# Kernel tuning notes

Hardware: AMD Instinct MI355X
Metric: run time of the kernel (lower is better)

Reference implementation:

```python
import jax, jax.numpy as jnp
import numpy as np

N, C_IN, C_OUT, C_REL, T, V = 64, 256, 256, 32, 64, 25

def conv1x1(x, w, b):
    # x: (n, ci, a, b), w: (co, ci), b: (co,) -> (n, co, a, b)
    return jnp.einsum('oc,ncab->noab', w, x) + b[None, :, None, None]

def setup_inputs() -> dict:
    key = jax.random.key(0)
    ks = jax.random.split(key, 10)
    s_in = 1.0 / np.sqrt(C_IN)
    s_rel = 1.0 / np.sqrt(C_REL)
    return {
        'x': jax.random.normal(ks[0], (N, C_IN, T, V), dtype=jnp.float32),
        'A': jax.random.normal(ks[1], (V, V), dtype=jnp.float32),
        'w1': jax.random.uniform(ks[2], (C_REL, C_IN), jnp.float32, -s_in, s_in),
        'b1': jax.random.uniform(ks[3], (C_REL,), jnp.float32, -s_in, s_in),
        'w2': jax.random.uniform(ks[4], (C_REL, C_IN), jnp.float32, -s_in, s_in),
        'b2': jax.random.uniform(ks[5], (C_REL,), jnp.float32, -s_in, s_in),
        'w3': jax.random.uniform(ks[6], (C_OUT, C_IN), jnp.float32, -s_in, s_in),
        'b3': jax.random.uniform(ks[7], (C_OUT,), jnp.float32, -s_in, s_in),
        'w4': jax.random.uniform(ks[8], (C_OUT, C_REL), jnp.float32, -s_rel, s_rel),
        'b4': jax.random.uniform(ks[9], (C_OUT,), jnp.float32, -s_rel, s_rel),
        'threhold': 0,
        'alpha': 1,
    }

def reference(x, A, w1, b1, w2, b2, w3, b3, w4, b4, threhold, alpha):
    # x: (n, c, t, v)
    # pooled 1x1 convs: fold the T-mean before the channel mix (linear ops commute)
    xm = x.mean(-2)                                   # (n, c, v)
    x1 = jnp.einsum('oc,ncv->nov', w1, xm) + b1[None, :, None]   # (n, r, v)
    x2 = jnp.einsum('oc,ncv->nov', w2, xm) + b2[None, :, None]   # (n, r, v)
    x3 = conv1x1(x, w3, b3)                           # (n, co, t, v)
    # channel-wise affinity: outer difference + tanh -> (n, r, v, v)
    aff = jnp.tanh(x1[:, :, :, None] - x2[:, :, None, :])
    # 1x1 conv over rel channels, scale, add adjacency
    attn = jnp.einsum('or,nruv->nouv', w4, aff) + b4[None, :, None, None]
    attn = attn * alpha + A[None, None]               # (n, co, v, v)
    # graph conv contraction
    out = jnp.einsum('ncuv,nctu->nctv', attn, x3)     # (n, co, t, v)
    return out
```

## Files before the change

kernel.cpp:

```cpp
#include <hip/hip_runtime.h>

#define N_  64
#define CI  256
#define CO  256
#define CR  32
#define T_  64
#define V_  25
#define TV  (T_*V_)
#define VV  (V_*V_)
#define ATS 640

typedef __attribute__((ext_vector_type(8))) short bshort8;
typedef __attribute__((ext_vector_type(4))) float f32x4;

__device__ inline unsigned short f2bf(float f) {
    unsigned int u = __float_as_uint(f);
    return (unsigned short)((u + 0x7FFFu + ((u >> 16) & 1u)) >> 16);
}

__global__ __launch_bounds__(256) void k_mean_cvt(const float* __restrict__ x,
                                                  const float* __restrict__ w3,
                                                  const float* __restrict__ w4,
                                                  float* __restrict__ xm,
                                                  unsigned short* __restrict__ w3f,
                                                  unsigned short* __restrict__ w4f) {
    int b = blockIdx.x;
    int tid = threadIdx.x;
    if (b < 1024) {
        __shared__ float L[16 * 400];
        int n = b >> 4, c0 = (b & 15) * 16;
        float a0 = 0.f, a1 = 0.f;
        for (int ch = 0; ch < 4; ++ch) {
            for (int i = 0; i < 7; ++i) {
                int task = i * 256 + tid;
                if (task < 1600) {
                    int c = task / 100, f4 = task % 100;
                    *(float4*)&L[c * 400 + f4 * 4] =
                        *(const float4*)(x + (size_t)(n * CI + c0 + c) * TV + ch * 400 + f4 * 4);
                }
            }
            __syncthreads();
            {
                int c = tid / 25, v = tid % 25;
                float s = 0.f;
                #pragma unroll
                for (int tl = 0; tl < 16; ++tl) s += L[c * 400 + tl * 25 + v];
                a0 += s;
            }
            if (tid < 144) {
                int oi = tid + 256;
                int c = oi / 25, v = oi % 25;
                float s = 0.f;
                #pragma unroll
                for (int tl = 0; tl < 16; ++tl) s += L[c * 400 + tl * 25 + v];
                a1 += s;
            }
            __syncthreads();
        }
        xm[(size_t)(n * CI + c0) * V_ + tid] = a0 * (1.f / T_);
        if (tid < 144)
            xm[(size_t)(n * CI + c0) * V_ + tid + 256] = a1 * (1.f / T_);
    } else if (b < 1056) {
        int f = (b - 1024) * 256 + tid;
        int lane = f & 63;
        int ks = (f >> 6) & 7;
        int ot = f >> 9;
        const float* src = w3 + (size_t)(ot * 16 + (lane & 15)) * CI + ks * 32 + (lane >> 4) * 8;
        bshort8 v;
        #pragma unroll
        for (int i = 0; i < 8; ++i) v[i] = (short)f2bf(src[i]);
        *(bshort8*)(w3f + (size_t)f * 8) = v;
    } else {
        int f = (b - 1056) * 256 + tid;
        int lane = f & 63;
        int ot = f >> 6;
        const float* src = w4 + (size_t)(ot * 16 + (lane & 15)) * CR + (lane >> 4) * 8;
        bshort8 v;
        #pragma unroll
        for (int i = 0; i < 8; ++i) v[i] = (short)f2bf(src[i]);
        *(bshort8*)(w4f + (size_t)f * 8) = v;
    }
}

__global__ __launch_bounds__(256) void k_x1x2(const float* __restrict__ xm,
                                              const float* __restrict__ w1,
                                              const float* __restrict__ b1,
                                              const float* __restrict__ w2,
                                              const float* __restrict__ b2,
                                              float* __restrict__ x1,
                                              float* __restrict__ x2) {
    int n = blockIdx.x, q = blockIdx.y;
    __shared__ float s_xm[CI * V_];
    const float4* src = (const float4*)(xm + (size_t)n * CI * V_);
    for (int i = threadIdx.x; i < CI * V_ / 4; i += 256) ((float4*)s_xm)[i] = src[i];
    __syncthreads();
    if (threadIdx.x < 200) {
        int idx = q * 200 + threadIdx.x;
        int r = idx / V_, v = idx % V_;
        const float* wr1 = w1 + (size_t)r * CI;
        const float* wr2 = w2 + (size_t)r * CI;
        float p1a = 0.f, p1b = 0.f, p2a = 0.f, p2b = 0.f;
        #pragma unroll 4
        for (int c = 0; c < CI; c += 2) {
            float xv0 = s_xm[c * V_ + v];
            float xv1 = s_xm[(c + 1) * V_ + v];
            p1a += wr1[c] * xv0;  p1b += wr1[c + 1] * xv1;
            p2a += wr2[c] * xv0;  p2b += wr2[c + 1] * xv1;
        }
        x1[n * CR * V_ + idx] = p1a + p1b + b1[r];
        x2[n * CR * V_ + idx] = p2a + p2b + b2[r];
    }
}

__global__ __launch_bounds__(256) void k_attn_gemm(const float* __restrict__ x,
                                                   const unsigned short* __restrict__ w3f,
                                                   const float* __restrict__ b3,
                                                   unsigned short* __restrict__ x3,
                                                   const float* __restrict__ x1,
                                                   const float* __restrict__ x2,
                                                   const unsigned short* __restrict__ w4f,
                                                   const float* __restrict__ b4,
                                                   const float* __restrict__ A,
                                                   const int* __restrict__ alpha_p,
                                                   unsigned short* __restrict__ attnT) {
    __shared__ __align__(16) unsigned char smem[32768];
    int tid = threadIdx.x;
    int bb  = blockIdx.x;
    if (bb >= 512) {
        unsigned short* sB = (unsigned short*)smem;
        int bg = bb - 512;
        int n = bg / 25, j0 = (bg % 25) * 64;
        int lane = tid & 63, wave = tid >> 6;
        const float* gx = x + (size_t)n * CI * TV + j0;
        for (int i = 0; i < 16; ++i) {
            int task = i * 256 + tid;
            int c = task >> 4, chunk = task & 15;
            float4 v = *(const float4*)(gx + (size_t)c * TV + chunk * 4);
            int g0 = c >> 3, cl = c & 7;
            #pragma unroll
            for (int k = 0; k < 4; ++k) {
                int j = chunk * 4 + k;
                int f = g0 ^ (j & 7) ^ ((j >> 2) & 7);
                float val = (k == 0) ? v.x : (k == 1) ? v.y : (k == 2) ? v.z : v.w;
                sB[j * 256 + f * 8 + cl] = f2bf(val);
            }
        }
        __syncthreads();
        int quad = lane >> 4, c16 = lane & 15;
        const bshort8* Af = (const bshort8*)w3f;
        f32x4 acc[4][4];
        #pragma unroll
        for (int mt = 0; mt < 4; ++mt)
            #pragma unroll
            for (int nt = 0; nt < 4; ++nt) acc[mt][nt] = (f32x4){0,0,0,0};
        #pragma unroll
        for (int ks = 0; ks < 8; ++ks) {
            bshort8 b[4], a[4];
            #pragma unroll
            for (int nt = 0; nt < 4; ++nt) {
                int rB = nt * 16 + c16;
                int cidx = ks * 4 + quad;
                int f = cidx ^ (rB & 7) ^ ((rB >> 2) & 7);
                b[nt] = *(const bshort8*)(&sB[rB * 256 + f * 8]);
            }
            #pragma unroll
            for (int mt = 0; mt < 4; ++mt)
                a[mt] = Af[(size_t)(((wave * 4 + mt) * 8 + ks) * 64) + lane];
            #pragma unroll
            for (int mt = 0; mt < 4; ++mt)
                #pragma unroll
                for (int nt = 0; nt < 4; ++nt)
                    acc[mt][nt] = __builtin_amdgcn_mfma_f32_16x16x32_bf16(a[mt], b[nt], acc[mt][nt], 0, 0, 0);
        }
        __syncthreads();
        unsigned short* eS = sB;
        #pragma unroll
        for (int pass = 0; pass < 2; ++pass) {
            if ((wave >> 1) == pass) {
                #pragma unroll
                for (int mt = 0; mt < 4; ++mt) {
                    int o = wave * 64 + mt * 16 + quad * 4;
                    float4 bvv = *(const float4*)(b3 + o);
                    int ol = (wave & 1) * 64 + mt * 16 + quad * 4;
                    #pragma unroll
                    for (int nt = 0; nt < 4; ++nt) {
                        int jc = nt * 16 + c16;
                        eS[(ol + 0) * 72 + jc] = f2bf(acc[mt][nt][0] + bvv.x);
                        eS[(ol + 1) * 72 + jc] = f2bf(acc[mt][nt][1] + bvv.y);
                        eS[(ol + 2) * 72 + jc] = f2bf(acc[mt][nt][2] + bvv.z);
                        eS[(ol + 3) * 72 + jc] = f2bf(acc[mt][nt][3] + bvv.w);
                    }
                }
            }
            __syncthreads();
            #pragma unroll
            for (int i = 0; i < 4; ++i) {
                int task = i * 256 + tid;
                int orow = task >> 3, seg = task & 7;
                bshort8 vv = *(const bshort8*)&eS[orow * 72 + seg * 8];
                *(bshort8*)(x3 + (size_t)(n * CO + pass * 128 + orow) * TV + j0 + seg * 8) = vv;
            }
            __syncthreads();
        }
    } else {
        float* s_x1 = (float*)smem;
        float* s_x2 = s_x1 + CR * V_;
        float* s_A  = s_x2 + CR * V_;
        int n = bb >> 3, by = bb & 7;
        float alpha = (float)alpha_p[0];
        for (int i = tid; i < CR * V_; i += 256) {
            s_x1[i] = x1[n * CR * V_ + i];
            s_x2[i] = x2[n * CR * V_ + i];
        }
        for (int i = tid; i < VV; i += 256) s_A[i] = A[i];
        __syncthreads();
        int wave = tid >> 6, lane = tid & 63;
        int task = by * 4 + wave;
        int og   = task & 3;
        int ug   = task >> 2;
        int o0   = og * 64;
        int quad = lane >> 4, c16 = lane & 15;
        bshort8 a[4];
        #pragma unroll
        for (int ot = 0; ot < 4; ++ot)
            a[ot] = *(const bshort8*)(w4f + (size_t)(((og * 4) + ot) * 64 + lane) * 8);
        float4 bv[4];
        #pragma unroll
        for (int ot = 0; ot < 4; ++ot)
            bv[ot] = *(const float4*)(b4 + o0 + ot * 16 + quad * 4);
        int r0 = quad * 8;
        #pragma unroll
        for (int it = 0; it < 5; ++it) {
            int uv0 = (ug * 5 + it) * 16;
            int uvc = uv0 + c16;
            bool valid = uvc < VV;
            int uvcc = valid ? uvc : (VV - 1);
            int u = uvcc % V_, v = uvcc / V_;
            bshort8 b;
            #pragma unroll
            for (int i = 0; i < 8; ++i) {
                float d = s_x1[(r0 + i) * V_ + u] - s_x2[(r0 + i) * V_ + v];
                b[i] = (short)f2bf(tanhf(d));
            }
            float Auv = s_A[u * V_ + v];
            f32x4 acc[4];
            #pragma unroll
            for (int ot = 0; ot < 4; ++ot)
                acc[ot] = __builtin_amdgcn_mfma_f32_16x16x32_bf16(a[ot], b, (f32x4){0,0,0,0}, 0, 0, 0);
            if (valid) {
                #pragma unroll
                for (int ot = 0; ot < 4; ++ot) {
                    #pragma unroll
                    for (int r = 0; r < 4; ++r) {
                        int o = o0 + ot * 16 + quad * 4 + r;
                        float bval = (r == 0) ? bv[ot].x : (r == 1) ? bv[ot].y
                                   : (r == 2) ? bv[ot].z : bv[ot].w;
                        attnT[(size_t)(n * CO + o) * ATS + uvc] =
                            f2bf((acc[ot][r] + bval) * alpha + Auv);
                    }
                }
            }
        }
    }
}

__global__ __launch_bounds__(256) void k_contract(const unsigned short* __restrict__ x3,
                                                  const unsigned short* __restrict__ attnT,
                                                  float* __restrict__ out) {
    int no0 = blockIdx.x * 4;
    __shared__ __align__(16) unsigned char smem[24576];
    unsigned short* sA = (unsigned short*)smem;
    unsigned short* sB = (unsigned short*)(smem + 16384);
    int tid = threadIdx.x;
    #pragma unroll
    for (int i = 0; i < 7; ++i) {
        int task = i * 256 + tid;
        if (task < 1792) {
            int p = task / 448, rem = task % 448;
            sA[p * 2048 + (rem / 7) * 32 + 25 + rem % 7] = 0;
        }
    }
    {
        int task = tid;
        for (int i = 0; i < 3; ++i, task += 256)
            if (task < 700) {
                int p = task / 175, rem = task % 175;
                sB[p * 1024 + (rem / 7) * 32 + 25 + rem % 7] = 0;
            }
    }
    #pragma unroll
    for (int i = 0; i < 4; ++i) {
        int task = i * 256 + tid;
        if (task < 800) {
            int p = task / 200, e8 = task % 200;
            bshort8 vv = *(const bshort8*)(x3 + (size_t)(no0 + p) * TV + e8 * 8);
            #pragma unroll
            for (int k = 0; k < 8; ++k) {
                int j = e8 * 8 + k;
                int t = j / 25, u = j % 25;
                sA[p * 2048 + t * 32 + u] = (unsigned short)vv[k];
            }
        }
    }
    #pragma unroll
    for (int i = 0; i < 2; ++i) {
        int task = i * 256 + tid;
        if (task < 316) {
            int p = task / 79, e8 = task % 79;
            bshort8 vv = *(const bshort8*)(attnT + (size_t)(no0 + p) * ATS + e8 * 8);
            #pragma unroll
            for (int k = 0; k < 8; ++k) {
                int idx = e8 * 8 + k;
                if (idx < VV) {
                    int v = idx / 25, u = idx % 25;
                    sB[p * 1024 + v * 32 + u] = (unsigned short)vv[k];
                }
            }
        }
    }
    __syncthreads();
    int p = tid >> 6, lane = tid & 63;
    int quad = lane >> 4, c16 = lane & 15;
    const unsigned short* pA = sA + p * 2048;
    const unsigned short* pB = sB + p * 1024;
    bshort8 a[4], b[2];
    #pragma unroll
    for (int mt = 0; mt < 4; ++mt) a[mt] = *(const bshort8*)&pA[(mt * 16 + c16) * 32 + quad * 8];
    #pragma unroll
    for (int nt = 0; nt < 2; ++nt) b[nt] = *(const bshort8*)&pB[(nt * 16 + c16) * 32 + quad * 8];
    f32x4 acc[4][2];
    #pragma unroll
    for (int mt = 0; mt < 4; ++mt)
        #pragma unroll
        for (int nt = 0; nt < 2; ++nt)
            acc[mt][nt] = __builtin_amdgcn_mfma_f32_16x16x32_bf16(a[mt], b[nt], (f32x4){0,0,0,0}, 0, 0, 0);
    size_t ob = (size_t)(no0 + p) * TV;
    #pragma unroll
    for (int mt = 0; mt < 4; ++mt)
        #pragma unroll
        for (int nt = 0; nt < 2; ++nt) {
            int v = nt * 16 + c16;
            if (v < V_) {
                #pragma unroll
                for (int r = 0; r < 4; ++r) {
                    int t = mt * 16 + quad * 4 + r;
                    out[ob + t * 25 + v] = acc[mt][nt][r];
                }
            }
        }
}

extern "C" void kernel_launch(void* const* d_in, const int* in_sizes, int n_in,
                              void* d_out, int out_size, void* d_ws, size_t ws_size,
                              hipStream_t stream) {
    const float* x  = (const float*)d_in[0];
    const float* A  = (const float*)d_in[1];
    const float* w1 = (const float*)d_in[2];
    const float* b1 = (const float*)d_in[3];
    const float* w2 = (const float*)d_in[4];
    const float* b2 = (const float*)d_in[5];
    const float* w3 = (const float*)d_in[6];
    const float* b3 = (const float*)d_in[7];
    const float* w4 = (const float*)d_in[8];
    const float* b4 = (const float*)d_in[9];
    const int* alpha_p = (const int*)d_in[11];
    float* out = (float*)d_out;

    float* ws = (float*)d_ws;
    float* xm = ws;
    float* x1 = ws + 409600;
    float* x2 = ws + 460800;
    unsigned short* attnT = (unsigned short*)(ws + 512000);
    unsigned short* w3f   = attnT + (size_t)16384 * ATS;
    unsigned short* w4f   = w3f + 65536;
    unsigned short* x3    = w4f + 16384;

    k_mean_cvt<<<1060, 256, 0, stream>>>(x, w3, w4, xm, w3f, w4f);
    k_x1x2<<<dim3(N_, 4), 256, 0, stream>>>(xm, w1, b1, w2, b2, x1, x2);
    k_attn_gemm<<<2112, 256, 0, stream>>>(x, w3f, b3, x3, x1, x2, w4f, b4, A, alpha_p, attnT);
    k_contract<<<4096, 256, 0, stream>>>(x3, attnT, out);
}
```

Measured before the change: 298.6 us.

## Emit x3 in padded MFMA-ready layout so contraction loads fragments directly

```diff
diff --git a/kernel.cpp b/kernel.cpp
--- a/kernel.cpp
+++ b/kernel.cpp
@@ -9,6 +9,7 @@
 #define TV  (T_*V_)
 #define VV  (V_*V_)
 #define ATS 640
+#define XPS 2048
 
 typedef __attribute__((ext_vector_type(8))) short bshort8;
 typedef __attribute__((ext_vector_type(4))) float f32x4;
@@ -115,7 +116,7 @@
 __global__ __launch_bounds__(256) void k_attn_gemm(const float* __restrict__ x,
                                                    const unsigned short* __restrict__ w3f,
                                                    const float* __restrict__ b3,
-                                                   unsigned short* __restrict__ x3,
+                                                   unsigned short* __restrict__ x3p,
                                                    const float* __restrict__ x1,
                                                    const float* __restrict__ x2,
                                                    const unsigned short* __restrict__ w4f,
@@ -126,22 +127,22 @@
     __shared__ __align__(16) unsigned char smem[32768];
     int tid = threadIdx.x;
     int bb  = blockIdx.x;
-    if (bb >= 512) {
+    if (bb < 2048) {
         unsigned short* sB = (unsigned short*)smem;
-        int bg = bb - 512;
-        int n = bg / 25, j0 = (bg % 25) * 64;
+        int n = bb >> 5, jt = bb & 31;
+        int j0 = jt * 50;
         int lane = tid & 63, wave = tid >> 6;
         const float* gx = x + (size_t)n * CI * TV + j0;
-        for (int i = 0; i < 16; ++i) {
+        for (int i = 0; i < 25; ++i) {
             int task = i * 256 + tid;
-            int c = task >> 4, chunk = task & 15;
-            float4 v = *(const float4*)(gx + (size_t)c * TV + chunk * 4);
+            int c = task / 25, f2 = task % 25;
+            float2 v = *(const float2*)(gx + (size_t)c * TV + f2 * 2);
             int g0 = c >> 3, cl = c & 7;
             #pragma unroll
-            for (int k = 0; k < 4; ++k) {
-                int j = chunk * 4 + k;
+            for (int k = 0; k < 2; ++k) {
+                int j = f2 * 2 + k;
                 int f = g0 ^ (j & 7) ^ ((j >> 2) & 7);
-                float val = (k == 0) ? v.x : (k == 1) ? v.y : (k == 2) ? v.z : v.w;
+                float val = (k == 0) ? v.x : v.y;
                 sB[j * 256 + f * 8 + cl] = f2bf(val);
             }
         }
@@ -184,12 +185,23 @@
                     int ol = (wave & 1) * 64 + mt * 16 + quad * 4;
                     #pragma unroll
                     for (int nt = 0; nt < 4; ++nt) {
-                        int jc = nt * 16 + c16;
-                        eS[(ol + 0) * 72 + jc] = f2bf(acc[mt][nt][0] + bvv.x);
-                        eS[(ol + 1) * 72 + jc] = f2bf(acc[mt][nt][1] + bvv.y);
-                        eS[(ol + 2) * 72 + jc] = f2bf(acc[mt][nt][2] + bvv.z);
-                        eS[(ol + 3) * 72 + jc] = f2bf(acc[mt][nt][3] + bvv.w);
+                        int j = nt * 16 + c16;
+                        if (j < 50) {
+                            int tl = j / 25, u = j % 25;
+                            int off = tl * 32 + u;
+                            eS[(ol + 0) * 72 + off] = f2bf(acc[mt][nt][0] + bvv.x);
+                            eS[(ol + 1) * 72 + off] = f2bf(acc[mt][nt][1] + bvv.y);
+                            eS[(ol + 2) * 72 + off] = f2bf(acc[mt][nt][2] + bvv.z);
+                            eS[(ol + 3) * 72 + off] = f2bf(acc[mt][nt][3] + bvv.w);
+                        }
                     }
+                }
+            } else if (pass == 0) {
+                int q = (wave & 1) * 64 + lane;
+                #pragma unroll
+                for (int u = 25; u < 32; ++u) {
+                    eS[q * 72 + u] = 0;
+                    eS[q * 72 + 32 + u] = 0;
                 }
             }
             __syncthreads();
@@ -198,7 +210,7 @@
                 int task = i * 256 + tid;
                 int orow = task >> 3, seg = task & 7;
                 bshort8 vv = *(const bshort8*)&eS[orow * 72 + seg * 8];
-                *(bshort8*)(x3 + (size_t)(n * CO + pass * 128 + orow) * TV + j0 + seg * 8) = vv;
+                *(bshort8*)(x3p + (size_t)(n * CO + pass * 128 + orow) * XPS + jt * 64 + seg * 8) = vv;
             }
             __syncthreads();
         }
@@ -206,7 +218,8 @@
         float* s_x1 = (float*)smem;
         float* s_x2 = s_x1 + CR * V_;
         float* s_A  = s_x2 + CR * V_;
-        int n = bb >> 3, by = bb & 7;
+        int b2 = bb - 2048;
+        int n = b2 >> 3, by = b2 & 7;
         float alpha = (float)alpha_p[0];
         for (int i = tid; i < CR * V_; i += 256) {
             s_x1[i] = x1[n * CR * V_ + i];
@@ -264,68 +277,46 @@
     }
 }
 
-__global__ __launch_bounds__(256) void k_contract(const unsigned short* __restrict__ x3,
+__global__ __launch_bounds__(256) void k_contract(const unsigned short* __restrict__ x3p,
                                                   const unsigned short* __restrict__ attnT,
                                                   float* __restrict__ out) {
     int no0 = blockIdx.x * 4;
-    __shared__ __align__(16) unsigned char smem[24576];
-    unsigned short* sA = (unsigned short*)smem;
-    unsigned short* sB = (unsigned short*)(smem + 16384);
+    __shared__ __align__(16) unsigned short sB[4 * 1024];
     int tid = threadIdx.x;
-    #pragma unroll
-    for (int i = 0; i < 7; ++i) {
-        int task = i * 256 + tid;
-        if (task < 1792) {
-            int p = task / 448, rem = task % 448;
-            sA[p * 2048 + (rem / 7) * 32 + 25 + rem % 7] = 0;
-        }
-    }
+    int p = tid >> 6, lane = tid & 63;
+    int quad = lane >> 4, c16 = lane & 15;
+    const unsigned short* pAg = x3p + (size_t)(no0 + p) * XPS;
+    bshort8 a[4];
+    #pragma unroll
+    for (int mt = 0; mt < 4; ++mt)
+        a[mt] = *(const bshort8*)(pAg + (size_t)(mt * 16 + c16) * 32 + quad * 8);
     {
         int task = tid;
         for (int i = 0; i < 3; ++i, task += 256)
             if (task < 700) {
-                int p = task / 175, rem = task % 175;
-                sB[p * 1024 + (rem / 7) * 32 + 25 + rem % 7] = 0;
-            }
-    }
-    #pragma unroll
-    for (int i = 0; i < 4; ++i) {
-        int task = i * 256 + tid;
-        if (task < 800) {
-            int p = task / 200, e8 = task % 200;
-            bshort8 vv = *(const bshort8*)(x3 + (size_t)(no0 + p) * TV + e8 * 8);
-            #pragma unroll
-            for (int k = 0; k < 8; ++k) {
-                int j = e8 * 8 + k;
-                int t = j / 25, u = j % 25;
-                sA[p * 2048 + t * 32 + u] = (unsigned short)vv[k];
-            }
-        }
+                int pp = task / 175, rem = task % 175;
+                sB[pp * 1024 + (rem / 7) * 32 + 25 + rem % 7] = 0;
+            }
     }
     #pragma unroll
     for (int i = 0; i < 2; ++i) {
         int task = i * 256 + tid;
         if (task < 316) {
-            int p = task / 79, e8 = task % 79;
-            bshort8 vv = *(const bshort8*)(attnT + (size_t)(no0 + p) * ATS + e8 * 8);
+            int pp = task / 79, e8 = task % 79;
+            bshort8 vv = *(const bshort8*)(attnT + (size_t)(no0 + pp) * ATS + e8 * 8);
             #pragma unroll
             for (int k = 0; k < 8; ++k) {
                 int idx = e8 * 8 + k;
                 if (idx < VV) {
                     int v = idx / 25, u = idx % 25;
-                    sB[p * 1024 + v * 32 + u] = (unsigned short)vv[k];
+                    sB[pp * 1024 + v * 32 + u] = (unsigned short)vv[k];
                 }
             }
         }
     }
     __syncthreads();
-    int p = tid >> 6, lane = tid & 63;
-    int quad = lane >> 4, c16 = lane & 15;
-    const unsigned short* pA = sA + p * 2048;
     const unsigned short* pB = sB + p * 1024;
-    bshort8 a[4], b[2];
-    #pragma unroll
-    for (int mt = 0; mt < 4; ++mt) a[mt] = *(const bshort8*)&pA[(mt * 16 + c16) * 32 + quad * 8];
+    bshort8 b[2];
     #pragma unroll
     for (int nt = 0; nt < 2; ++nt) b[nt] = *(const bshort8*)&pB[(nt * 16 + c16) * 32 + quad * 8];
     f32x4 acc[4][2];
@@ -373,10 +364,10 @@
     unsigned short* attnT = (unsigned short*)(ws + 512000);
     unsigned short* w3f   = attnT + (size_t)16384 * ATS;
     unsigned short* w4f   = w3f + 65536;
-    unsigned short* x3    = w4f + 16384;
+    unsigned short* x3p   = w4f + 16384;
 
     k_mean_cvt<<<1060, 256, 0, stream>>>(x, w3, w4, xm, w3f, w4f);
     k_x1x2<<<dim3(N_, 4), 256, 0, stream>>>(xm, w1, b1, w2, b2, x1, x2);
-    k_attn_gemm<<<2112, 256, 0, stream>>>(x, w3f, b3, x3, x1, x2, w4f, b4, A, alpha_p, attnT);
-    k_contract<<<4096, 256, 0, stream>>>(x3, attnT, out);
-}
+    k_attn_gemm<<<2560, 256, 0, stream>>>(x, w3f, b3, x3p, x1, x2, w4f, b4, A, alpha_p, attnT);
+    k_contract<<<4096, 256, 0, stream>>>(x3p, attnT, out);
+}
```

New measurement: 319.1 us. +6.9%, slower.
